# Optimization experiments

Hardware: AMD Instinct MI355X
Metric: run time of the kernel (lower is better)

The kernel has to match this reference:

```python
import jax, jax.numpy as jnp
import numpy as np

B, S, D = 4, 2048, 1024
H = 16
HD = D // H  # 64


def setup_inputs() -> dict:
    key = jax.random.key(0)
    ks = jax.random.split(key, 5)
    s = 0.02
    return {
        "x": jax.random.normal(ks[0], (B, S, D), dtype=jnp.float32),
        "w_qkv": jax.random.normal(ks[1], (D, 3 * D), dtype=jnp.float32) * s,
        "b_qkv": jnp.zeros((3 * D,), dtype=jnp.float32),
        "w_out": jax.random.normal(ks[2], (D, D), dtype=jnp.float32) * s,
        "b_out": jnp.zeros((D,), dtype=jnp.float32),
    }


def reference(x, w_qkv, b_qkv, w_out, b_out):
    b, s, d = x.shape
    qkv = x @ w_qkv + b_qkv                              # [b,s,3d]
    qkv = qkv.reshape(b, s, 3, H, HD)
    q = qkv[:, :, 0].transpose(0, 2, 1, 3)               # [b,h,s,hd]
    k = qkv[:, :, 1].transpose(0, 2, 1, 3)
    v = qkv[:, :, 2].transpose(0, 2, 1, 3)
    scale = 1.0 / jnp.sqrt(jnp.asarray(HD, dtype=x.dtype))
    scores = jnp.einsum("bhqd,bhkd->bhqk", q, k) * scale  # [b,h,s,s]
    causal = jnp.tril(jnp.ones((s, s), dtype=bool))
    scores = jnp.where(causal[None, None], scores, jnp.asarray(-jnp.inf, dtype=x.dtype))
    probs = jax.nn.softmax(scores, axis=-1)
    out = jnp.einsum("bhqk,bhkd->bhqd", probs, v)        # [b,h,s,hd]
    out = out.transpose(0, 2, 1, 3).reshape(b, s, d)
    return out @ w_out + b_out
```

## Files before the change

kernel.cpp:

```cpp
#include <hip/hip_runtime.h>
#include <hip/hip_bf16.h>

typedef __bf16 bf16_t;
typedef __bf16 bf16x4 __attribute__((ext_vector_type(4)));
typedef __bf16 bf16x8 __attribute__((ext_vector_type(8)));
typedef float f32x4 __attribute__((ext_vector_type(4)));

#define Bb 4
#define Ss 2048
#define Dd 1024
#define Hh 16
#define HDd 64

#define QSC 0.1803368801111244f

__device__ __forceinline__ void gld16(const bf16_t* g, bf16_t* l) {
  __builtin_amdgcn_global_load_lds(
      (const __attribute__((address_space(1))) unsigned int*)g,
      (__attribute__((address_space(3))) unsigned int*)l, 16, 0, 0);
}

__global__ __launch_bounds__(256) void conv_to_bf16(
    const float* __restrict__ src, bf16_t* __restrict__ dst) {
  int i = (blockIdx.x * 256 + threadIdx.x) * 4;
  float4 v = *(const float4*)&src[i];
  bf16x4 o = {(bf16_t)v.x, (bf16_t)v.y, (bf16_t)v.z, (bf16_t)v.w};
  *(bf16x4*)&dst[i] = o;
}

__global__ __launch_bounds__(256) void transpose_conv(
    const float* __restrict__ in, bf16_t* __restrict__ out, int R, int C) {
  __shared__ bf16_t tile[32][33];
  int c0 = blockIdx.x * 32, r0 = blockIdx.y * 32;
  int tx = threadIdx.x, ty = threadIdx.y;
#pragma unroll
  for (int j = 0; j < 32; j += 8)
    tile[ty + j][tx] = (bf16_t)in[(size_t)(r0 + ty + j) * C + c0 + tx];
  __syncthreads();
#pragma unroll
  for (int j = 0; j < 32; j += 8)
    out[(size_t)(c0 + ty + j) * R + r0 + tx] = tile[tx][ty + j];
}

template <int MODE>
__global__ __launch_bounds__(256) void gemm_mfma(
    const bf16_t* __restrict__ A, const bf16_t* __restrict__ Bt,
    const float* __restrict__ bias, float* __restrict__ outf,
    bf16_t* __restrict__ out0, bf16_t* __restrict__ out1,
    bf16_t* __restrict__ out2, int M, int N, int K) {
  const int tid = threadIdx.x;
  const int lane = tid & 63;
  const int wave = tid >> 6;
  const int quad = lane >> 4;
  const int lr = lane & 15;
  const int wr = wave >> 1;
  const int wc = wave & 1;
  const int m0 = blockIdx.y * 128;
  const int n0 = blockIdx.x * 128;

  __shared__ __align__(16) bf16_t As[128 * 32];
  __shared__ __align__(16) bf16_t Bs[128 * 32];

  const f32x4 zero = {0.f, 0.f, 0.f, 0.f};
  f32x4 acc[4][4];
#pragma unroll
  for (int mi = 0; mi < 4; ++mi)
#pragma unroll
    for (int ni = 0; ni < 4; ++ni) acc[mi][ni] = zero;

  for (int kt = 0; kt < K; kt += 32) {
#pragma unroll
    for (int i = 0; i < 2; ++i) {
      int chunk = tid + i * 256;
      int row = chunk >> 2;
      int c8 = (chunk & 3) * 8;
      gld16(&A[(size_t)(m0 + row) * K + kt + c8], &As[chunk * 8]);
      gld16(&Bt[(size_t)(n0 + row) * K + kt + c8], &Bs[chunk * 8]);
    }
    __syncthreads();
    bf16x8 af[4], bfr[4];
    const int k0 = quad * 8;
#pragma unroll
    for (int mi = 0; mi < 4; ++mi)
      af[mi] = *(const bf16x8*)&As[(wr * 64 + mi * 16 + lr) * 32 + k0];
#pragma unroll
    for (int ni = 0; ni < 4; ++ni)
      bfr[ni] = *(const bf16x8*)&Bs[(wc * 64 + ni * 16 + lr) * 32 + k0];
#pragma unroll
    for (int mi = 0; mi < 4; ++mi)
#pragma unroll
      for (int ni = 0; ni < 4; ++ni)
        acc[mi][ni] = __builtin_amdgcn_mfma_f32_16x16x32_bf16(
            af[mi], bfr[ni], acc[mi][ni], 0, 0, 0);
    __syncthreads();
  }

#pragma unroll
  for (int mi = 0; mi < 4; ++mi) {
    const int mbase = m0 + wr * 64 + mi * 16 + quad * 4;
#pragma unroll
    for (int ni = 0; ni < 4; ++ni) {
      const int n = n0 + wc * 64 + ni * 16 + lr;
      const float bv = bias[n];
      if (MODE == 1) {
#pragma unroll
        for (int r = 0; r < 4; ++r)
          outf[(size_t)(mbase + r) * N + n] = acc[mi][ni][r] + bv;
      } else {
        const int which = n >> 10;
        const int h = (n >> 6) & 15;
        const int hd = n & 63;
        const int b = mbase >> 11;
        const int s = mbase & 2047;
        if (which == 2) {
          bf16x4 pk = {(bf16_t)(acc[mi][ni][0] + bv),
                       (bf16_t)(acc[mi][ni][1] + bv),
                       (bf16_t)(acc[mi][ni][2] + bv),
                       (bf16_t)(acc[mi][ni][3] + bv)};
          *(bf16x4*)&out2[(((size_t)(b * Hh + h)) * HDd + hd) * Ss + s] = pk;
        } else {
          bf16_t* dst = (which == 0) ? out0 : out1;
          const float sc = (which == 0) ? QSC : 1.0f;
#pragma unroll
          for (int r = 0; r < 4; ++r)
            dst[(((size_t)(b * Hh + h)) * Ss + s + r) * HDd + hd] =
                (bf16_t)((acc[mi][ni][r] + bv) * sc);
        }
      }
    }
  }
}

__global__ __launch_bounds__(256) void attn_kernel(
    const bf16_t* __restrict__ Qg, const bf16_t* __restrict__ Kg,
    const bf16_t* __restrict__ Vtg, bf16_t* __restrict__ Og) {
  const int tid = threadIdx.x;
  const int lane = tid & 63;
  const int wave = tid >> 6;
  const int quad = lane >> 4;
  const int lr = lane & 15;

  const int bid = blockIdx.x;
  const int xcd = bid & 7;
  const int j = bid >> 3;
  const int bh = xcd * 8 + (j >> 3);
  const int p = j & 7;
  const int b = bh >> 4;
  const int h = bh & 15;
  const int wq = wave * 32;

  const bf16_t* Qp = Qg + (size_t)bh * Ss * HDd;
  const bf16_t* Kp = Kg + (size_t)bh * Ss * HDd;
  const bf16_t* Vp = Vtg + (size_t)bh * HDd * Ss;

  __shared__ bf16_t Ks[2][64 * 72];
  __shared__ bf16_t Vts[2][64 * 72];
  __shared__ bf16_t Ps[4][32 * 72];

  bf16x8 kreg[2], vreg[2];
  const int r0 = tid >> 3;
  const int c0 = (tid & 7) * 8;

  const f32x4 zero = {0.f, 0.f, 0.f, 0.f};

#pragma unroll
  for (int i = 0; i < 2; ++i) {
    kreg[i] = *(const bf16x8*)&Kp[(size_t)(r0 + i * 32) * HDd + c0];
    vreg[i] = *(const bf16x8*)&Vp[(size_t)(r0 + i * 32) * Ss + c0];
  }

  int cur = 0;
  for (int half = 0; half < 2; ++half) {
    const int qt = half ? p : 15 - p;
    const int qbase = qt * 128;
    const int ktiles = qt * 2 + 2;

    bf16x8 bq[2][2];
#pragma unroll
    for (int qt2 = 0; qt2 < 2; ++qt2)
#pragma unroll
      for (int kk2 = 0; kk2 < 2; ++kk2)
        bq[qt2][kk2] = *(const bf16x8*)&Qp[(size_t)(qbase + wq + qt2 * 16 +
                                                    lr) *
                                               HDd +
                                           kk2 * 32 + quad * 8];

    f32x4 oacc[4][2];
#pragma unroll
    for (int dt = 0; dt < 4; ++dt)
#pragma unroll
      for (int qt2 = 0; qt2 < 2; ++qt2) oacc[dt][qt2] = zero;
    float l_run[2] = {0.f, 0.f};

    for (int kt = 0; kt < ktiles; ++kt) {
      const int kbase = kt * 64;

#pragma unroll
      for (int i = 0; i < 2; ++i) {
        *(bf16x8*)&Ks[cur][(r0 + i * 32) * 72 + c0] = kreg[i];
        *(bf16x8*)&Vts[cur][(r0 + i * 32) * 72 + c0] = vreg[i];
      }
      __syncthreads();

      const int nkb = (kt + 1 < ktiles) ? kbase + 64 : 0;
#pragma unroll
      for (int i = 0; i < 2; ++i) {
        kreg[i] = *(const bf16x8*)&Kp[(size_t)(nkb + r0 + i * 32) * HDd + c0];
        vreg[i] = *(const bf16x8*)&Vp[(size_t)(r0 + i * 32) * Ss + nkb + c0];
      }

      f32x4 sacc[4][2];
#pragma unroll
      for (int kt4 = 0; kt4 < 4; ++kt4)
#pragma unroll
        for (int qt2 = 0; qt2 < 2; ++qt2) sacc[kt4][qt2] = zero;
#pragma unroll
      for (int kk2 = 0; kk2 < 2; ++kk2) {
        bf16x8 ak[4];
#pragma unroll
        for (int kt4 = 0; kt4 < 4; ++kt4)
          ak[kt4] = *(const bf16x8*)&Ks[cur][(kt4 * 16 + lr) * 72 + kk2 * 32 +
                                             quad * 8];
#pragma unroll
        for (int kt4 = 0; kt4 < 4; ++kt4)
#pragma unroll
          for (int qt2 = 0; qt2 < 2; ++qt2)
            sacc[kt4][qt2] = __builtin_amdgcn_mfma_f32_16x16x32_bf16(
                ak[kt4], bq[qt2][kk2], sacc[kt4][qt2], 0, 0, 0);
      }

      const bool edge = (kt >= 2 * qt);
#pragma unroll
      for (int kt4 = 0; kt4 < 4; ++kt4)
#pragma unroll
        for (int qt2 = 0; qt2 < 2; ++qt2)
#pragma unroll
          for (int r = 0; r < 4; ++r) {
            float s = sacc[kt4][qt2][r];
            if (edge) {
              const int qg = qbase + wq + qt2 * 16 + lr;
              const int kg = kbase + kt4 * 16 + quad * 4 + r;
              if (kg > qg) s = -1e30f;
            }
            const float pv = __builtin_amdgcn_exp2f(s);
            sacc[kt4][qt2][r] = pv;
            l_run[qt2] += pv;
          }

#pragma unroll
      for (int kt4 = 0; kt4 < 4; ++kt4)
#pragma unroll
        for (int qt2 = 0; qt2 < 2; ++qt2) {
          bf16x4 pk = {(bf16_t)sacc[kt4][qt2][0], (bf16_t)sacc[kt4][qt2][1],
                       (bf16_t)sacc[kt4][qt2][2], (bf16_t)sacc[kt4][qt2][3]};
          *(bf16x4*)&Ps[wave][(qt2 * 16 + lr) * 72 + kt4 * 16 + quad * 4] = pk;
        }

#pragma unroll
      for (int kk2 = 0; kk2 < 2; ++kk2) {
        bf16x8 av[4], bp[2];
#pragma unroll
        for (int dt = 0; dt < 4; ++dt)
          av[dt] = *(const bf16x8*)&Vts[cur][(dt * 16 + lr) * 72 + kk2 * 32 +
                                             quad * 8];
#pragma unroll
        for (int qt2 = 0; qt2 < 2; ++qt2)
          bp[qt2] = *(const bf16x8*)&Ps[wave][(qt2 * 16 + lr) * 72 + kk2 * 32 +
                                              quad * 8];
#pragma unroll
        for (int dt = 0; dt < 4; ++dt)
#pragma unroll
          for (int qt2 = 0; qt2 < 2; ++qt2)
            oacc[dt][qt2] = __builtin_amdgcn_mfma_f32_16x16x32_bf16(
                av[dt], bp[qt2], oacc[dt][qt2], 0, 0, 0);
      }
      cur ^= 1;
    }

#pragma unroll
    for (int qt2 = 0; qt2 < 2; ++qt2) {
      l_run[qt2] += __shfl_xor(l_run[qt2], 16, 64);
      l_run[qt2] += __shfl_xor(l_run[qt2], 32, 64);
    }

#pragma unroll
    for (int qt2 = 0; qt2 < 2; ++qt2) {
      const float inv = 1.f / l_run[qt2];
      const int qg = qbase + wq + qt2 * 16 + lr;
#pragma unroll
      for (int dt = 0; dt < 4; ++dt) {
        bf16x4 ov = {(bf16_t)(oacc[dt][qt2][0] * inv),
                     (bf16_t)(oacc[dt][qt2][1] * inv),
                     (bf16_t)(oacc[dt][qt2][2] * inv),
                     (bf16_t)(oacc[dt][qt2][3] * inv)};
        *(bf16x4*)&Og[((size_t)b * Ss + qg) * Dd + h * HDd + dt * 16 +
                      quad * 4] = ov;
      }
    }
  }
}

extern "C" void kernel_launch(void* const* d_in, const int* in_sizes, int n_in,
                              void* d_out, int out_size, void* d_ws,
                              size_t ws_size, hipStream_t stream) {
  const float* x = (const float*)d_in[0];
  const float* w_qkv = (const float*)d_in[1];
  const float* b_qkv = (const float*)d_in[2];
  const float* w_out = (const float*)d_in[3];
  const float* b_out = (const float*)d_in[4];
  float* out = (float*)d_out;

  bf16_t* Kb = (bf16_t*)d_ws;
  bf16_t* Vt = Kb + (size_t)Bb * Hh * Ss * HDd;
  bf16_t* slot3 = Vt + (size_t)Bb * Hh * Ss * HDd;
  bf16_t* Wt1 = slot3;
  bf16_t* Ob = slot3;
  bf16_t* Wt2 = Kb;
  bf16_t* Qb = (bf16_t*)d_out;
  bf16_t* Xc = (bf16_t*)d_out + (size_t)8192 * 1024;

  conv_to_bf16<<<8192, 256, 0, stream>>>(x, Xc);
  transpose_conv<<<dim3(96, 32), dim3(32, 8), 0, stream>>>(w_qkv, Wt1, 1024,
                                                           3072);

  gemm_mfma<0><<<dim3(24, 64), 256, 0, stream>>>(
      Xc, Wt1, b_qkv, nullptr, Qb, Kb, Vt, 8192, 3072, 1024);

  attn_kernel<<<dim3(512), 256, 0, stream>>>(Qb, Kb, Vt, Ob);

  transpose_conv<<<dim3(32, 32), dim3(32, 8), 0, stream>>>(w_out, Wt2, 1024,
                                                           1024);

  gemm_mfma<1><<<dim3(8, 64), 256, 0, stream>>>(
      Ob, Wt2, b_out, out, nullptr, nullptr, nullptr, 8192, 1024, 1024);
}
```

Baseline: 273.0 us.

## Add 256x256-tile 8-wave GEMM with 4-stage pipeline for QKV projection

Adds a new GEMM kernel with 512 threads (8 waves) computing 256x256 output tiles. It uses a 4-deep LDS ring buffer filled by direct global-to-LDS loads and splits each K-step into two MFMA halves, interleaving the A and B prefetches with compute. Wave priority is raised around the MFMA bursts. The QKV projection now uses it instead of the 128-tile kernel, aiming for more operand reuse per loaded byte and better latency hiding. The cost is a large LDS footprint (128KB per block) and higher register pressure, which limit occupancy. The grid also shrinks to 384 blocks.

```diff
diff --git a/kernel.cpp b/kernel.cpp
--- a/kernel.cpp
+++ b/kernel.cpp
@@ -131,6 +131,135 @@
   }
 }
 
+template <int MODE>
+__global__ __launch_bounds__(512, 2) void gemm_mfma8(
+    const bf16_t* __restrict__ A, const bf16_t* __restrict__ Bt,
+    const float* __restrict__ bias, float* __restrict__ outf,
+    bf16_t* __restrict__ out0, bf16_t* __restrict__ out1,
+    bf16_t* __restrict__ out2, int M, int N, int K) {
+  const int tid = threadIdx.x;
+  const int lane = tid & 63;
+  const int wave = tid >> 6;
+  const int quad = lane >> 4;
+  const int lr = lane & 15;
+  const int wr = wave >> 2;
+  const int wc = wave & 3;
+  const int m0 = blockIdx.y * 256;
+  const int n0 = blockIdx.x * 256;
+
+  __shared__ __align__(16) bf16_t As[4][256 * 32];
+  __shared__ __align__(16) bf16_t Bs[4][256 * 32];
+
+  const f32x4 zero = {0.f, 0.f, 0.f, 0.f};
+  f32x4 acc[8][4];
+#pragma unroll
+  for (int m = 0; m < 8; ++m)
+#pragma unroll
+    for (int n = 0; n < 4; ++n) acc[m][n] = zero;
+
+  int srow[2], scol[2];
+#pragma unroll
+  for (int i = 0; i < 2; ++i) {
+    int c = tid + i * 512;
+    srow[i] = c >> 2;
+    scol[i] = ((c & 3) ^ ((srow[i] >> 1) & 3)) * 8;
+  }
+  const int nk = K >> 5;
+
+  auto stageA = [&](int t) {
+#pragma unroll
+    for (int i = 0; i < 2; ++i)
+      gld16(&A[(size_t)(m0 + srow[i]) * K + (t << 5) + scol[i]],
+            &As[t & 3][(tid + i * 512) * 8]);
+  };
+  auto stageB = [&](int t) {
+#pragma unroll
+    for (int i = 0; i < 2; ++i)
+      gld16(&Bt[(size_t)(n0 + srow[i]) * K + (t << 5) + scol[i]],
+            &Bs[t & 3][(tid + i * 512) * 8]);
+  };
+
+  stageA(0); stageB(0);
+  if (nk > 1) { stageA(1); stageB(1); }
+  if (nk > 2) { stageA(2); stageB(2); }
+  asm volatile("s_waitcnt vmcnt(8)" ::: "memory");
+  __builtin_amdgcn_s_barrier();
+
+  const int sw = (lr >> 1) & 3;
+  const int qx = (quad ^ sw) * 8;
+
+  for (int t = 0; t < nk; ++t) {
+    const bf16_t* as = As[t & 3];
+    const bf16_t* bs = Bs[t & 3];
+    bf16x8 af[4], bfr[4];
+#pragma unroll
+    for (int n = 0; n < 4; ++n)
+      bfr[n] = *(const bf16x8*)&bs[(wc * 64 + n * 16 + lr) * 32 + qx];
+#pragma unroll
+    for (int m = 0; m < 4; ++m)
+      af[m] = *(const bf16x8*)&as[(wr * 128 + m * 16 + lr) * 32 + qx];
+    if (t + 3 < nk) stageA(t + 3);
+    __builtin_amdgcn_s_setprio(1);
+#pragma unroll
+    for (int m = 0; m < 4; ++m)
+#pragma unroll
+      for (int n = 0; n < 4; ++n)
+        acc[m][n] = __builtin_amdgcn_mfma_f32_16x16x32_bf16(af[m], bfr[n],
+                                                            acc[m][n], 0, 0, 0);
+    __builtin_amdgcn_s_setprio(0);
+    __builtin_amdgcn_s_barrier();
+#pragma unroll
+    for (int m = 0; m < 4; ++m)
+      af[m] = *(const bf16x8*)&as[(wr * 128 + (m + 4) * 16 + lr) * 32 + qx];
+    if (t + 3 < nk) stageB(t + 3);
+    __builtin_amdgcn_s_setprio(1);
+#pragma unroll
+    for (int m = 0; m < 4; ++m)
+#pragma unroll
+      for (int n = 0; n < 4; ++n)
+        acc[m + 4][n] = __builtin_amdgcn_mfma_f32_16x16x32_bf16(
+            af[m], bfr[n], acc[m + 4][n], 0, 0, 0);
+    __builtin_amdgcn_s_setprio(0);
+    asm volatile("s_waitcnt vmcnt(8)" ::: "memory");
+    __builtin_amdgcn_s_barrier();
+  }
+
+#pragma unroll
+  for (int mi = 0; mi < 8; ++mi) {
+    const int mbase = m0 + wr * 128 + mi * 16 + quad * 4;
+#pragma unroll
+    for (int ni = 0; ni < 4; ++ni) {
+      const int n = n0 + wc * 64 + ni * 16 + lr;
+      const float bv = bias[n];
+      if (MODE == 1) {
+#pragma unroll
+        for (int r = 0; r < 4; ++r)
+          outf[(size_t)(mbase + r) * N + n] = acc[mi][ni][r] + bv;
+      } else {
+        const int which = n >> 10;
+        const int h = (n >> 6) & 15;
+        const int hd = n & 63;
+        const int b = mbase >> 11;
+        const int s = mbase & 2047;
+        if (which == 2) {
+          bf16x4 pk = {(bf16_t)(acc[mi][ni][0] + bv),
+                       (bf16_t)(acc[mi][ni][1] + bv),
+                       (bf16_t)(acc[mi][ni][2] + bv),
+                       (bf16_t)(acc[mi][ni][3] + bv)};
+          *(bf16x4*)&out2[(((size_t)(b * Hh + h)) * HDd + hd) * Ss + s] = pk;
+        } else {
+          bf16_t* dst = (which == 0) ? out0 : out1;
+          const float sc = (which == 0) ? QSC : 1.0f;
+#pragma unroll
+          for (int r = 0; r < 4; ++r)
+            dst[(((size_t)(b * Hh + h)) * Ss + s + r) * HDd + hd] =
+                (bf16_t)((acc[mi][ni][r] + bv) * sc);
+        }
+      }
+    }
+  }
+}
+
 __global__ __launch_bounds__(256) void attn_kernel(
     const bf16_t* __restrict__ Qg, const bf16_t* __restrict__ Kg,
     const bf16_t* __restrict__ Vtg, bf16_t* __restrict__ Og) {
@@ -323,7 +452,7 @@
   transpose_conv<<<dim3(96, 32), dim3(32, 8), 0, stream>>>(w_qkv, Wt1, 1024,
                                                            3072);
 
-  gemm_mfma<0><<<dim3(24, 64), 256, 0, stream>>>(
+  gemm_mfma8<0><<<dim3(12, 32), 512, 0, stream>>>(
       Xc, Wt1, b_qkv, nullptr, Qb, Kb, Vt, 8192, 3072, 1024);
 
   attn_kernel<<<dim3(512), 256, 0, stream>>>(Qb, Kb, Vt, Ob);
```

Result: no change. 268.8 us (-1.5%).

## Pipeline GEMM with three-stage LDS ring, larger M tile, and XOR swizzle

Applied to the files above, without the earlier changes.

Rewrites the bf16 MFMA GEMM used for the QKV and output projections. A triple-buffered LDS ring with vmcnt-based waits keeps two K-tiles of global-to-LDS loads in flight while the current tile is computed, and it drops one of the two barriers per iteration. The block tile grows to 256x128 so each wave does 8x4 MFMAs, raising reuse of each LDS fragment. An XOR swizzle on LDS columns is meant to reduce bank conflicts, and setprio raises priority around the MFMA burst. The cost is higher register and LDS use (the launch bound asks for 2 blocks per SM) and half as many blocks, which could hurt occupancy or load balance.

```diff
diff --git a/kernel.cpp b/kernel.cpp
--- a/kernel.cpp
+++ b/kernel.cpp
@@ -43,7 +43,7 @@
 }
 
 template <int MODE>
-__global__ __launch_bounds__(256) void gemm_mfma(
+__global__ __launch_bounds__(256, 2) void gemm_ring(
     const bf16_t* __restrict__ A, const bf16_t* __restrict__ Bt,
     const float* __restrict__ bias, float* __restrict__ outf,
     bf16_t* __restrict__ out0, bf16_t* __restrict__ out1,
@@ -55,49 +55,94 @@
   const int lr = lane & 15;
   const int wr = wave >> 1;
   const int wc = wave & 1;
-  const int m0 = blockIdx.y * 128;
+  const int m0 = blockIdx.y * 256;
   const int n0 = blockIdx.x * 128;
 
-  __shared__ __align__(16) bf16_t As[128 * 32];
-  __shared__ __align__(16) bf16_t Bs[128 * 32];
+  __shared__ __align__(16) bf16_t As[3][256 * 32];
+  __shared__ __align__(16) bf16_t Bs[3][128 * 32];
 
   const f32x4 zero = {0.f, 0.f, 0.f, 0.f};
-  f32x4 acc[4][4];
-#pragma unroll
-  for (int mi = 0; mi < 4; ++mi)
+  f32x4 acc[8][4];
+#pragma unroll
+  for (int mi = 0; mi < 8; ++mi)
 #pragma unroll
     for (int ni = 0; ni < 4; ++ni) acc[mi][ni] = zero;
 
-  for (int kt = 0; kt < K; kt += 32) {
-#pragma unroll
-    for (int i = 0; i < 2; ++i) {
-      int chunk = tid + i * 256;
-      int row = chunk >> 2;
-      int c8 = (chunk & 3) * 8;
-      gld16(&A[(size_t)(m0 + row) * K + kt + c8], &As[chunk * 8]);
-      gld16(&Bt[(size_t)(n0 + row) * K + kt + c8], &Bs[chunk * 8]);
-    }
-    __syncthreads();
-    bf16x8 af[4], bfr[4];
-    const int k0 = quad * 8;
-#pragma unroll
-    for (int mi = 0; mi < 4; ++mi)
-      af[mi] = *(const bf16x8*)&As[(wr * 64 + mi * 16 + lr) * 32 + k0];
+  int ar[4], ac[4], br[2], bc[2];
+#pragma unroll
+  for (int i = 0; i < 4; ++i) {
+    int c = tid + i * 256;
+    ar[i] = c >> 2;
+    ac[i] = ((c & 3) ^ ((ar[i] >> 1) & 3)) * 8;
+  }
+#pragma unroll
+  for (int i = 0; i < 2; ++i) {
+    int c = tid + i * 256;
+    br[i] = c >> 2;
+    bc[i] = ((c & 3) ^ ((br[i] >> 1) & 3)) * 8;
+  }
+
+  const int nk = K >> 5;
+
+  auto stage = [&](int t, int s) {
+    const int ko = t << 5;
+#pragma unroll
+    for (int i = 0; i < 4; ++i)
+      gld16(&A[(size_t)(m0 + ar[i]) * K + ko + ac[i]],
+            &As[s][(tid + i * 256) * 8]);
+#pragma unroll
+    for (int i = 0; i < 2; ++i)
+      gld16(&Bt[(size_t)(n0 + br[i]) * K + ko + bc[i]],
+            &Bs[s][(tid + i * 256) * 8]);
+  };
+
+  stage(0, 0);
+  if (nk > 1) {
+    stage(1, 1);
+    asm volatile("s_waitcnt vmcnt(6)" ::: "memory");
+  } else {
+    asm volatile("s_waitcnt vmcnt(0)" ::: "memory");
+  }
+  __builtin_amdgcn_s_barrier();
+
+  const int qx = (quad ^ ((lr >> 1) & 3)) * 8;
+
+  int scur = 0;
+  for (int t = 0; t < nk; ++t) {
+    const bool more2 = (t + 2 < nk);
+    if (more2) {
+      int s2 = scur + 2;
+      if (s2 >= 3) s2 -= 3;
+      stage(t + 2, s2);
+    }
+    bf16x8 af[8], bfr[4];
+#pragma unroll
+    for (int mi = 0; mi < 8; ++mi)
+      af[mi] = *(const bf16x8*)&As[scur][(wr * 128 + mi * 16 + lr) * 32 + qx];
 #pragma unroll
     for (int ni = 0; ni < 4; ++ni)
-      bfr[ni] = *(const bf16x8*)&Bs[(wc * 64 + ni * 16 + lr) * 32 + k0];
-#pragma unroll
-    for (int mi = 0; mi < 4; ++mi)
+      bfr[ni] = *(const bf16x8*)&Bs[scur][(wc * 64 + ni * 16 + lr) * 32 + qx];
+    __builtin_amdgcn_s_setprio(1);
+#pragma unroll
+    for (int mi = 0; mi < 8; ++mi)
 #pragma unroll
       for (int ni = 0; ni < 4; ++ni)
         acc[mi][ni] = __builtin_amdgcn_mfma_f32_16x16x32_bf16(
             af[mi], bfr[ni], acc[mi][ni], 0, 0, 0);
-    __syncthreads();
-  }
-
-#pragma unroll
-  for (int mi = 0; mi < 4; ++mi) {
-    const int mbase = m0 + wr * 64 + mi * 16 + quad * 4;
+    __builtin_amdgcn_s_setprio(0);
+    if (t + 1 < nk) {
+      if (more2)
+        asm volatile("s_waitcnt vmcnt(6)" ::: "memory");
+      else
+        asm volatile("s_waitcnt vmcnt(0)" ::: "memory");
+      __builtin_amdgcn_s_barrier();
+    }
+    scur = (scur == 2) ? 0 : scur + 1;
+  }
+
+#pragma unroll
+  for (int mi = 0; mi < 8; ++mi) {
+    const int mbase = m0 + wr * 128 + mi * 16 + quad * 4;
 #pragma unroll
     for (int ni = 0; ni < 4; ++ni) {
       const int n = n0 + wc * 64 + ni * 16 + lr;
@@ -323,7 +368,7 @@
   transpose_conv<<<dim3(96, 32), dim3(32, 8), 0, stream>>>(w_qkv, Wt1, 1024,
                                                            3072);
 
-  gemm_mfma<0><<<dim3(24, 64), 256, 0, stream>>>(
+  gemm_ring<0><<<dim3(24, 32), 256, 0, stream>>>(
       Xc, Wt1, b_qkv, nullptr, Qb, Kb, Vt, 8192, 3072, 1024);
 
   attn_kernel<<<dim3(512), 256, 0, stream>>>(Qb, Kb, Vt, Ob);
@@ -331,6 +376,6 @@
   transpose_conv<<<dim3(32, 32), dim3(32, 8), 0, stream>>>(w_out, Wt2, 1024,
                                                            1024);
 
-  gemm_mfma<1><<<dim3(8, 64), 256, 0, stream>>>(
+  gemm_ring<1><<<dim3(8, 32), 256, 0, stream>>>(
       Ob, Wt2, b_out, out, nullptr, nullptr, nullptr, 8192, 1024, 1024);
 }
```

New measurement: 288.3 us. 1.06x slower.
